# Performance work log

Measured on AMD Instinct MI355X. Metric: run time of the kernel, lower is better.

## Reference

```python
import jax, jax.numpy as jnp
import numpy as np

EMBED_DIM = 768
NUM_HEADS = 12
HEAD_DIM = EMBED_DIM // NUM_HEADS


def setup_inputs() -> dict:
    key = jax.random.key(0)
    k1, k2, k3, k4, k5 = jax.random.split(key, 5)
    x = jax.random.normal(k1, (2, 4096, EMBED_DIM), dtype=jnp.float32)
    # nn.Linear(embedding_dim, 3*embedding_dim): weight [3d, d], bias [3d]
    w_qkv = jax.random.normal(k2, (3 * EMBED_DIM, EMBED_DIM), dtype=jnp.float32) * (1.0 / np.sqrt(EMBED_DIM))
    b_qkv = jax.random.normal(k3, (3 * EMBED_DIM,), dtype=jnp.float32) * 0.02
    # LayerNorm affine params
    ln_gamma = jnp.ones((EMBED_DIM,), dtype=jnp.float32)
    ln_beta = jnp.zeros((EMBED_DIM,), dtype=jnp.float32)
    return {"x": x, "w_qkv": w_qkv, "b_qkv": b_qkv, "ln_gamma": ln_gamma, "ln_beta": ln_beta}


def _layernorm(x, gamma, beta, eps=1e-5):
    mu = jnp.mean(x, axis=-1, keepdims=True)
    var = jnp.var(x, axis=-1, keepdims=True)
    return (x - mu) * jax.lax.rsqrt(var + eps) * gamma + beta


def reference(x, w_qkv, b_qkv, ln_gamma, ln_beta):
    b, n, d = x.shape
    h, hd = NUM_HEADS, HEAD_DIM
    qkv = x @ w_qkv.T + b_qkv                      # [b, n, 3d]
    qkv = qkv.reshape(b, n, 3, h, hd)
    qkv = jnp.transpose(qkv, (2, 0, 3, 1, 4))      # [3, b, h, n, hd]
    Q, K, V = qkv[0], qkv[1], qkv[2]
    scale = 1.0 / np.sqrt(hd).astype(np.float32)
    scores = jnp.einsum('bhqd,bhkd->bhqk', Q, K) * scale   # [b, h, n, n]
    attn = jax.nn.softmax(scores, axis=-1)
    out = jnp.einsum('bhqk,bhkd->bhqd', attn, V)           # [b, h, n, hd]
    out = jnp.transpose(out, (0, 2, 1, 3)).reshape(b, n, d)
    return _layernorm(x + out, ln_gamma, ln_beta)
```

## Files before the change

kernel.cpp:

```cpp
#include <hip/hip_runtime.h>
#include <stdint.h>

#define NUM_HEADS 12
#define HEAD_DIM 64
#define EMB 768
#define SEQ 4096
#define BATCH 2
#define ROWS (BATCH*SEQ)
#define DQKV (3*EMB)

typedef __attribute__((ext_vector_type(8))) __bf16 bf16x8;
typedef __attribute__((ext_vector_type(4))) float floatx4;

static __device__ __forceinline__ unsigned short f2bf(float f) {
  unsigned int u = __float_as_uint(f);
  u += 0x7FFFu + ((u >> 16) & 1u);
  return (unsigned short)(u >> 16);
}

static __device__ __forceinline__ unsigned int pack_bf2(float a, float b) {
  unsigned int u0 = __float_as_uint(a) + 0x8000u;
  unsigned int u1 = __float_as_uint(b) + 0x8000u;
  return __builtin_amdgcn_perm(u1, u0, 0x07060302u);
}

static __device__ __forceinline__ void async_cp16(void* lds, const void* g) {
  __builtin_amdgcn_global_load_lds(
      (__attribute__((address_space(1))) void*)(g),
      (__attribute__((address_space(3))) void*)(lds), 16, 0, 0);
}

__global__ __launch_bounds__(256) void cvt_bf16_kernel(
    const float* __restrict__ src, unsigned short* __restrict__ dst, int n4) {
  int i = blockIdx.x * blockDim.x + threadIdx.x;
  if (i >= n4) return;
  float4 v = ((const float4*)src)[i];
  ushort4 o;
  o.x = f2bf(v.x); o.y = f2bf(v.y); o.z = f2bf(v.z); o.w = f2bf(v.w);
  ((ushort4*)dst)[i] = o;
}

__global__ __launch_bounds__(256) void qkv_gemm_kernel(
    const unsigned short* __restrict__ xb, const unsigned short* __restrict__ wb,
    const float* __restrict__ bias,
    unsigned short* __restrict__ Qb, unsigned short* __restrict__ Kb,
    unsigned short* __restrict__ Vt) {
  __shared__ unsigned short As[128 * 64];
  __shared__ unsigned short Bs[128 * 64];
  const int t = threadIdx.x;
  const int lane = t & 63;
  const int w = t >> 6;
  const int wm = w >> 1, wn = w & 1;
  const int fr = lane & 15, fq = lane >> 4;
  const int fx = fr & 7;
  const int m0 = blockIdx.x * 128;
  const int n0 = blockIdx.y * 128;
  const int lr = t >> 3;
  const int sc = t & 7;

  floatx4 acc[4][4];
#pragma unroll
  for (int i = 0; i < 4; ++i)
#pragma unroll
    for (int j = 0; j < 4; ++j) acc[i][j] = (floatx4)(0.0f);

  for (int k0 = 0; k0 < EMB; k0 += 64) {
    __syncthreads();
#pragma unroll
    for (int i = 0; i < 4; ++i) {
      const int rr = i*32 + lr;
      const int cg = ((sc ^ (lr & 7)) * 8);
      async_cp16(&As[rr*64 + sc*8], &xb[(size_t)(m0 + rr)*EMB + k0 + cg]);
      async_cp16(&Bs[rr*64 + sc*8], &wb[(size_t)(n0 + rr)*EMB + k0 + cg]);
    }
    __syncthreads();
#pragma unroll
    for (int ks = 0; ks < 2; ++ks) {
      bf16x8 af[4], bfr[4];
#pragma unroll
      for (int i = 0; i < 4; ++i)
        af[i] = *(const bf16x8*)&As[(wm*64 + i*16 + fr)*64 + (((ks*4+fq) ^ fx)*8)];
#pragma unroll
      for (int j = 0; j < 4; ++j)
        bfr[j] = *(const bf16x8*)&Bs[(wn*64 + j*16 + fr)*64 + (((ks*4+fq) ^ fx)*8)];
#pragma unroll
      for (int i = 0; i < 4; ++i)
#pragma unroll
        for (int j = 0; j < 4; ++j)
          acc[i][j] = __builtin_amdgcn_mfma_f32_16x16x32_bf16(af[i], bfr[j], acc[i][j], 0, 0, 0);
    }
  }

  const int sel = n0 / EMB;
  const float qscale = 0.125f * 1.4426950408889634f;
#pragma unroll
  for (int i = 0; i < 4; ++i) {
    const int mbase = m0 + wm*64 + i*16 + fq*4;
    const int b = mbase / SEQ;
    const int nn = mbase - b*SEQ;
#pragma unroll
    for (int j = 0; j < 4; ++j) {
      const int og = n0 + wn*64 + j*16 + fr;
      const int oo = og - sel*EMB;
      const int hh = oo >> 6, dd = oo & 63;
      const float bv = bias[og];
      if (sel == 2) {
        ushort4 pk;
        pk.x = f2bf(acc[i][j][0] + bv);
        pk.y = f2bf(acc[i][j][1] + bv);
        pk.z = f2bf(acc[i][j][2] + bv);
        pk.w = f2bf(acc[i][j][3] + bv);
        *(ushort4*)&Vt[(((size_t)(b*NUM_HEADS + hh))*HEAD_DIM + dd)*SEQ + nn] = pk;
      } else {
        unsigned short* dst = (sel == 0) ? Qb : Kb;
        const float sc2 = (sel == 0) ? qscale : 1.0f;
        const size_t base = (((size_t)(b*NUM_HEADS + hh))*SEQ + nn)*HEAD_DIM + dd;
#pragma unroll
        for (int r = 0; r < 4; ++r)
          dst[base + (size_t)r*HEAD_DIM] = f2bf((acc[i][j][r] + bv) * sc2);
      }
    }
  }
}

__global__ __launch_bounds__(256, 3) void attn_kernel(
    const unsigned short* __restrict__ Qb, const unsigned short* __restrict__ Kb,
    const unsigned short* __restrict__ Vt, float* __restrict__ Oo) {
  __shared__ unsigned short Ks[128 * 64];
  __shared__ unsigned short Vs[64 * 128];
  const int t = threadIdx.x;
  const int lane = t & 63;
  const int w = t >> 6;
  const int fr = lane & 15, fq = lane >> 4;
  const int fx = fr & 7;
  const int bh = blockIdx.y;
  const int q0 = blockIdx.x * 128 + w * 32;

  bf16x8 aq[2][2];
#pragma unroll
  for (int g = 0; g < 2; ++g) {
    const size_t qoff = ((size_t)bh * SEQ + q0 + g*16 + fr) * HEAD_DIM;
    aq[g][0] = *(const bf16x8*)&Qb[qoff + fq*8];
    aq[g][1] = *(const bf16x8*)&Qb[qoff + 32 + fq*8];
  }

  floatx4 o[2][4];
#pragma unroll
  for (int g = 0; g < 2; ++g)
#pragma unroll
    for (int d = 0; d < 4; ++d) o[g][d] = (floatx4)(0.f);
  float rs[2] = {0.f, 0.f};

  const size_t kb = (size_t)bh * SEQ * HEAD_DIM;
  const size_t vb = (size_t)bh * HEAD_DIM * SEQ;

  for (int kc = 0; kc < SEQ; kc += 128) {
    __syncthreads();
#pragma unroll
    for (int i = 0; i < 4; ++i) {
      const int chunk = i*256 + t;
      const int r = chunk >> 3, c = chunk & 7;
      async_cp16(&Ks[chunk*8], &Kb[kb + (size_t)(kc + r)*HEAD_DIM + ((c ^ (r&7))*8)]);
    }
#pragma unroll
    for (int i = 0; i < 4; ++i) {
      const int chunk = i*256 + t;
      const int r = chunk >> 4, c = chunk & 15;
      async_cp16(&Vs[chunk*8], &Vt[vb + (size_t)r*SEQ + kc + ((c ^ (r&7))*8)]);
    }
    __syncthreads();

#pragma unroll
    for (int J = 0; J < 4; ++J) {
      floatx4 z[2][2];
#pragma unroll
      for (int jj = 0; jj < 2; ++jj) {
        const int row = (J*2 + jj)*16 + fr;
        bf16x8 k0 = *(const bf16x8*)&Ks[row*64 + ((fq ^ fx)*8)];
        bf16x8 k1 = *(const bf16x8*)&Ks[row*64 + (((fq+4) ^ fx)*8)];
#pragma unroll
        for (int g = 0; g < 2; ++g) {
          floatx4 accz = (floatx4)(0.f);
          accz = __builtin_amdgcn_mfma_f32_16x16x32_bf16(k0, aq[g][0], accz, 0, 0, 0);
          accz = __builtin_amdgcn_mfma_f32_16x16x32_bf16(k1, aq[g][1], accz, 0, 0, 0);
          z[g][jj] = accz;
        }
      }
      bf16x8 ap[2];
#pragma unroll
      for (int g = 0; g < 2; ++g) {
        float e0 = __builtin_amdgcn_exp2f(z[g][0][0]);
        float e1 = __builtin_amdgcn_exp2f(z[g][0][1]);
        float e2 = __builtin_amdgcn_exp2f(z[g][0][2]);
        float e3 = __builtin_amdgcn_exp2f(z[g][0][3]);
        float e4 = __builtin_amdgcn_exp2f(z[g][1][0]);
        float e5 = __builtin_amdgcn_exp2f(z[g][1][1]);
        float e6 = __builtin_amdgcn_exp2f(z[g][1][2]);
        float e7 = __builtin_amdgcn_exp2f(z[g][1][3]);
        rs[g] += ((e0 + e1) + (e2 + e3)) + ((e4 + e5) + (e6 + e7));
        union { unsigned int u[4]; bf16x8 b; } cv;
        cv.u[0] = pack_bf2(e0, e1);
        cv.u[1] = pack_bf2(e2, e3);
        cv.u[2] = pack_bf2(e4, e5);
        cv.u[3] = pack_bf2(e6, e7);
        ap[g] = cv.b;
      }
#pragma unroll
      for (int dt = 0; dt < 4; ++dt) {
        const int r = dt*16 + fr;
        const int c0 = 4*J + (fq >> 1);
        const int c1 = c0 + 2;
        union { ushort4 h[2]; bf16x8 b; } vv;
        vv.h[0] = *(const ushort4*)&Vs[r*128 + ((c0 ^ fx)*8) + (fq&1)*4];
        vv.h[1] = *(const ushort4*)&Vs[r*128 + ((c1 ^ fx)*8) + (fq&1)*4];
#pragma unroll
        for (int g = 0; g < 2; ++g)
          o[g][dt] = __builtin_amdgcn_mfma_f32_16x16x32_bf16(ap[g], vv.b, o[g][dt], 0, 0, 0);
      }
    }
  }

#pragma unroll
  for (int g = 0; g < 2; ++g) {
    rs[g] += __shfl_xor(rs[g], 16);
    rs[g] += __shfl_xor(rs[g], 32);
  }
  const int b = bh / NUM_HEADS, hh = bh - b*NUM_HEADS;
#pragma unroll
  for (int g = 0; g < 2; ++g)
#pragma unroll
    for (int r4 = 0; r4 < 4; ++r4) {
      const float li = 1.0f / __shfl(rs[g], fq*4 + r4);
      const size_t obase = ((size_t)b*SEQ + q0 + g*16 + fq*4 + r4)*EMB + hh*HEAD_DIM;
#pragma unroll
      for (int dt = 0; dt < 4; ++dt)
        Oo[obase + dt*16 + fr] = o[g][dt][r4] * li;
    }
}

__global__ __launch_bounds__(256) void ln_kernel(
    const float* __restrict__ x, const float* __restrict__ att,
    const float* __restrict__ gamma, const float* __restrict__ beta,
    float* __restrict__ out) {
  const int row = blockIdx.x;
  const size_t base = (size_t)row * EMB;
  const int t = threadIdx.x;
  float v[3];
  float s = 0.f, s2 = 0.f;
#pragma unroll
  for (int k = 0; k < 3; ++k) {
    const int c = t + k*256;
    float val = x[base + c] + att[base + c];
    v[k] = val; s += val; s2 += val*val;
  }
#pragma unroll
  for (int off = 32; off > 0; off >>= 1) {
    s  += __shfl_down(s,  off);
    s2 += __shfl_down(s2, off);
  }
  __shared__ float red[8];
  if ((t & 63) == 0) { red[t >> 6] = s; red[4 + (t >> 6)] = s2; }
  __syncthreads();
  const float S  = red[0] + red[1] + red[2] + red[3];
  const float S2 = red[4] + red[5] + red[6] + red[7];
  const float mean = S * (1.0f / EMB);
  const float var  = S2 * (1.0f / EMB) - mean * mean;
  const float rstd = rsqrtf(var + 1e-5f);
#pragma unroll
  for (int k = 0; k < 3; ++k) {
    const int c = t + k*256;
    out[base + c] = (v[k] - mean) * rstd * gamma[c] + beta[c];
  }
}

extern "C" void kernel_launch(void* const* d_in, const int* in_sizes, int n_in,
                              void* d_out, int out_size, void* d_ws, size_t ws_size,
                              hipStream_t stream) {
  const float* x      = (const float*)d_in[0];
  const float* w_qkv  = (const float*)d_in[1];
  const float* b_qkv  = (const float*)d_in[2];
  const float* gamma  = (const float*)d_in[3];
  const float* beta   = (const float*)d_in[4];
  float* out = (float*)d_out;

  unsigned short* xb = (unsigned short*)d_ws;
  unsigned short* wb = xb + (size_t)ROWS * EMB;
  unsigned short* Qb = wb + (size_t)DQKV * EMB;
  unsigned short* Kb = Qb + (size_t)ROWS * EMB;
  unsigned short* Vt = Kb + (size_t)ROWS * EMB;
  float* att = (float*)(Vt + (size_t)ROWS * EMB);

  cvt_bf16_kernel<<<(ROWS*EMB/4 + 255)/256, 256, 0, stream>>>(x, xb, ROWS*EMB/4);
  cvt_bf16_kernel<<<(DQKV*EMB/4 + 255)/256, 256, 0, stream>>>(w_qkv, wb, DQKV*EMB/4);
  qkv_gemm_kernel<<<dim3(ROWS/128, DQKV/128), 256, 0, stream>>>(xb, wb, b_qkv, Qb, Kb, Vt);
  attn_kernel<<<dim3(SEQ/128, BATCH*NUM_HEADS), 256, 0, stream>>>(Qb, Kb, Vt, att);
  ln_kernel<<<ROWS, 256, 0, stream>>>(x, att, gamma, beta, out);
}
```

Measured before the change: 272.7 us.

## Compute softmax row sums via MFMA, store attention output as bf16, transpose GEMM epilogue

The attention kernel now gets the softmax denominator from an extra MFMA that multiplies the bf16 probabilities by a ones vector. This replaces the scalar adds and the final shuffles, and it makes the denominator use the same truncated bf16 values that feed the PV product. Probability packing switches from rounding to plain truncation. The attention output is written as bf16 instead of fp32, which halves that traffic, and layernorm widens it back to float. The QKV GEMM swaps its MFMA operands so that Q and K can be stored as packed ushort4 while V goes to scalar strided stores, and it loads bias as float4. These changes cost some precision.

Measured after the change: 258.6 us. 1.05x faster.

```diff
diff --git a/kernel.cpp b/kernel.cpp
--- a/kernel.cpp
+++ b/kernel.cpp
@@ -18,10 +18,8 @@
   return (unsigned short)(u >> 16);
 }
 
-static __device__ __forceinline__ unsigned int pack_bf2(float a, float b) {
-  unsigned int u0 = __float_as_uint(a) + 0x8000u;
-  unsigned int u1 = __float_as_uint(b) + 0x8000u;
-  return __builtin_amdgcn_perm(u1, u0, 0x07060302u);
+static __device__ __forceinline__ unsigned int pack_bf2_trunc(float a, float b) {
+  return __builtin_amdgcn_perm(__float_as_uint(b), __float_as_uint(a), 0x07060302u);
 }
 
 static __device__ __forceinline__ void async_cp16(void* lds, const void* g) {
@@ -87,37 +85,38 @@
       for (int i = 0; i < 4; ++i)
 #pragma unroll
         for (int j = 0; j < 4; ++j)
-          acc[i][j] = __builtin_amdgcn_mfma_f32_16x16x32_bf16(af[i], bfr[j], acc[i][j], 0, 0, 0);
+          acc[i][j] = __builtin_amdgcn_mfma_f32_16x16x32_bf16(bfr[j], af[i], acc[i][j], 0, 0, 0);
     }
   }
 
   const int sel = n0 / EMB;
   const float qscale = 0.125f * 1.4426950408889634f;
+  const float sc2 = (sel == 0) ? qscale : 1.0f;
 #pragma unroll
   for (int i = 0; i < 4; ++i) {
-    const int mbase = m0 + wm*64 + i*16 + fq*4;
-    const int b = mbase / SEQ;
-    const int nn = mbase - b*SEQ;
+    const int mr = m0 + wm*64 + i*16 + fr;
+    const int b = mr / SEQ;
+    const int nn = mr - b*SEQ;
 #pragma unroll
     for (int j = 0; j < 4; ++j) {
-      const int og = n0 + wn*64 + j*16 + fr;
+      const int og = n0 + wn*64 + j*16 + fq*4;
       const int oo = og - sel*EMB;
       const int hh = oo >> 6, dd = oo & 63;
-      const float bv = bias[og];
+      const float4 bv = *(const float4*)&bias[og];
       if (sel == 2) {
-        ushort4 pk;
-        pk.x = f2bf(acc[i][j][0] + bv);
-        pk.y = f2bf(acc[i][j][1] + bv);
-        pk.z = f2bf(acc[i][j][2] + bv);
-        pk.w = f2bf(acc[i][j][3] + bv);
-        *(ushort4*)&Vt[(((size_t)(b*NUM_HEADS + hh))*HEAD_DIM + dd)*SEQ + nn] = pk;
+        const size_t vtb = (((size_t)(b*NUM_HEADS + hh))*HEAD_DIM + dd)*SEQ + nn;
+        Vt[vtb + 0*SEQ] = f2bf(acc[i][j][0] + bv.x);
+        Vt[vtb + 1*SEQ] = f2bf(acc[i][j][1] + bv.y);
+        Vt[vtb + 2*SEQ] = f2bf(acc[i][j][2] + bv.z);
+        Vt[vtb + 3*SEQ] = f2bf(acc[i][j][3] + bv.w);
       } else {
         unsigned short* dst = (sel == 0) ? Qb : Kb;
-        const float sc2 = (sel == 0) ? qscale : 1.0f;
-        const size_t base = (((size_t)(b*NUM_HEADS + hh))*SEQ + nn)*HEAD_DIM + dd;
-#pragma unroll
-        for (int r = 0; r < 4; ++r)
-          dst[base + (size_t)r*HEAD_DIM] = f2bf((acc[i][j][r] + bv) * sc2);
+        ushort4 pk;
+        pk.x = f2bf((acc[i][j][0] + bv.x) * sc2);
+        pk.y = f2bf((acc[i][j][1] + bv.y) * sc2);
+        pk.z = f2bf((acc[i][j][2] + bv.z) * sc2);
+        pk.w = f2bf((acc[i][j][3] + bv.w) * sc2);
+        *(ushort4*)&dst[(((size_t)(b*NUM_HEADS + hh))*SEQ + nn)*HEAD_DIM + dd] = pk;
       }
     }
   }
@@ -125,7 +124,7 @@
 
 __global__ __launch_bounds__(256, 3) void attn_kernel(
     const unsigned short* __restrict__ Qb, const unsigned short* __restrict__ Kb,
-    const unsigned short* __restrict__ Vt, float* __restrict__ Oo) {
+    const unsigned short* __restrict__ Vt, unsigned short* __restrict__ Oo) {
   __shared__ unsigned short Ks[128 * 64];
   __shared__ unsigned short Vs[64 * 128];
   const int t = threadIdx.x;
@@ -144,12 +143,18 @@
     aq[g][1] = *(const bf16x8*)&Qb[qoff + 32 + fq*8];
   }
 
+  union { unsigned int u[4]; bf16x8 b; } onesu;
+  onesu.u[0] = onesu.u[1] = onesu.u[2] = onesu.u[3] = 0x3F803F80u;
+  const bf16x8 onesb = onesu.b;
+
   floatx4 o[2][4];
-#pragma unroll
-  for (int g = 0; g < 2; ++g)
+  floatx4 lsum[2];
+#pragma unroll
+  for (int g = 0; g < 2; ++g) {
+    lsum[g] = (floatx4)(0.f);
 #pragma unroll
     for (int d = 0; d < 4; ++d) o[g][d] = (floatx4)(0.f);
-  float rs[2] = {0.f, 0.f};
+  }
 
   const size_t kb = (size_t)bh * SEQ * HEAD_DIM;
   const size_t vb = (size_t)bh * HEAD_DIM * SEQ;
@@ -197,14 +202,16 @@
         float e5 = __builtin_amdgcn_exp2f(z[g][1][1]);
         float e6 = __builtin_amdgcn_exp2f(z[g][1][2]);
         float e7 = __builtin_amdgcn_exp2f(z[g][1][3]);
-        rs[g] += ((e0 + e1) + (e2 + e3)) + ((e4 + e5) + (e6 + e7));
         union { unsigned int u[4]; bf16x8 b; } cv;
-        cv.u[0] = pack_bf2(e0, e1);
-        cv.u[1] = pack_bf2(e2, e3);
-        cv.u[2] = pack_bf2(e4, e5);
-        cv.u[3] = pack_bf2(e6, e7);
+        cv.u[0] = pack_bf2_trunc(e0, e1);
+        cv.u[1] = pack_bf2_trunc(e2, e3);
+        cv.u[2] = pack_bf2_trunc(e4, e5);
+        cv.u[3] = pack_bf2_trunc(e6, e7);
         ap[g] = cv.b;
       }
+#pragma unroll
+      for (int g = 0; g < 2; ++g)
+        lsum[g] = __builtin_amdgcn_mfma_f32_16x16x32_bf16(ap[g], onesb, lsum[g], 0, 0, 0);
 #pragma unroll
       for (int dt = 0; dt < 4; ++dt) {
         const int r = dt*16 + fr;
@@ -220,26 +227,21 @@
     }
   }
 
-#pragma unroll
-  for (int g = 0; g < 2; ++g) {
-    rs[g] += __shfl_xor(rs[g], 16);
-    rs[g] += __shfl_xor(rs[g], 32);
-  }
   const int b = bh / NUM_HEADS, hh = bh - b*NUM_HEADS;
 #pragma unroll
   for (int g = 0; g < 2; ++g)
 #pragma unroll
     for (int r4 = 0; r4 < 4; ++r4) {
-      const float li = 1.0f / __shfl(rs[g], fq*4 + r4);
+      const float li = 1.0f / lsum[g][r4];
       const size_t obase = ((size_t)b*SEQ + q0 + g*16 + fq*4 + r4)*EMB + hh*HEAD_DIM;
 #pragma unroll
       for (int dt = 0; dt < 4; ++dt)
-        Oo[obase + dt*16 + fr] = o[g][dt][r4] * li;
+        Oo[obase + dt*16 + fr] = f2bf(o[g][dt][r4] * li);
     }
 }
 
 __global__ __launch_bounds__(256) void ln_kernel(
-    const float* __restrict__ x, const float* __restrict__ att,
+    const float* __restrict__ x, const unsigned short* __restrict__ att,
     const float* __restrict__ gamma, const float* __restrict__ beta,
     float* __restrict__ out) {
   const int row = blockIdx.x;
@@ -250,7 +252,8 @@
 #pragma unroll
   for (int k = 0; k < 3; ++k) {
     const int c = t + k*256;
-    float val = x[base + c] + att[base + c];
+    float a = __uint_as_float(((unsigned int)att[base + c]) << 16);
+    float val = x[base + c] + a;
     v[k] = val; s += val; s2 += val*val;
   }
 #pragma unroll
@@ -288,7 +291,7 @@
   unsigned short* Qb = wb + (size_t)DQKV * EMB;
   unsigned short* Kb = Qb + (size_t)ROWS * EMB;
   unsigned short* Vt = Kb + (size_t)ROWS * EMB;
-  float* att = (float*)(Vt + (size_t)ROWS * EMB);
+  unsigned short* att = Vt + (size_t)ROWS * EMB;
 
   cvt_bf16_kernel<<<(ROWS*EMB/4 + 255)/256, 256, 0, stream>>>(x, xb, ROWS*EMB/4);
   cvt_bf16_kernel<<<(DQKV*EMB/4 + 255)/256, 256, 0, stream>>>(w_qkv, wb, DQKV*EMB/4);
```
